# Kernel optimization log

Measured on AMD Instinct MI355X. Metric: run time of the kernel, lower is better.

Reference implementation:

```python
import jax, jax.numpy as jnp
import numpy as np

N, G, CIN, COUT, K, M, H, W = 4, 8, 256, 256, 3, 4, 32, 32


def setup_inputs() -> dict:
    key = jax.random.key(0)
    ks = jax.random.split(key, 12)
    s = 0.02
    return {
        "x": jax.random.normal(ks[0], (N, G, CIN, H, W), jnp.float32),
        # grouped 1x1 conv weights: (G, out_per_group, in_per_group)
        "wq": jax.random.normal(ks[1], (G, COUT, CIN), jnp.float32) * s,
        "wk": jax.random.normal(ks[2], (G, COUT, CIN), jnp.float32) * s,
        "wv": jax.random.normal(ks[3], (G, COUT, CIN), jnp.float32) * s,
        # relative embeddings: height varies over K1, width over K2
        "hm": jax.random.normal(ks[4], (G * COUT // 2, K, 1), jnp.float32),
        "wm": jax.random.normal(ks[5], (G * COUT // 2, 1, K), jnp.float32),
        "w_conv": jax.random.normal(ks[6], (G, CIN, COUT), jnp.float32) * s,
        "b_conv": jnp.zeros((G, CIN), jnp.float32),
        "w_f1": jax.random.normal(ks[7], (G, COUT, CIN), jnp.float32) * s,
        "b_f1": jnp.zeros((G, COUT), jnp.float32),
        "w_f2": jax.random.normal(ks[8], (G, CIN, COUT), jnp.float32) * s,
        "b_f2": jnp.zeros((G, CIN), jnp.float32),
        "g1": jnp.ones((CIN // M,), jnp.float32),
        "b1": jnp.zeros((CIN // M,), jnp.float32),
        "g2": jnp.ones((CIN // M,), jnp.float32),
        "b2": jnp.zeros((CIN // M,), jnp.float32),
    }


def _gconv(x, w, b=None):
    # grouped 1x1 conv: x (N,G,Ci,H,W), w (G,Co,Ci)
    y = jnp.einsum('ngihw,goi->ngohw', x, w)
    return y if b is None else y + b[None, :, :, None, None]


def _unfold(x4, k):
    # nn.Unfold(k, 1, (k-1)//2, 1): x4 (N,C,H,W) -> patches (N,C,k,k,H,W)
    p = (k - 1) // 2
    hh, ww = x4.shape[2], x4.shape[3]
    xp = jnp.pad(x4, ((0, 0), (0, 0), (p, p), (p, p)))
    return jnp.stack(
        [jnp.stack([xp[:, :, i:i + hh, j:j + ww] for j in range(k)], axis=2)
         for i in range(k)], axis=2)


def _skip(t, m):
    # 'N G (M D) H W -> N (H W) M G D'
    n, g, c, h, w = t.shape
    d = c // m
    return t.reshape(n, g, m, d, h, w).transpose(0, 4, 5, 2, 1, 3).reshape(n, h * w, m, g, d)


def _ln(t, gamma, beta, eps=1e-5):
    mu = t.mean(-1, keepdims=True)
    var = t.var(-1, keepdims=True)  # biased, matches torch LayerNorm
    return (t - mu) / jnp.sqrt(var + eps) * gamma + beta


def _forward(x, wq, wk, wv, hm, wm, w_conv, b_conv, w_f1, b_f1, w_f2, b_f2, g1, b1, g2, b2):
    n, g, c, h, w = x.shape
    m = M
    dout = COUT // m
    q = _gconv(x, wq).reshape(n, g, m, dout, h, w)
    k0 = _gconv(x, wk).reshape(n, g * COUT, h, w)
    kp = _unfold(k0, K)  # (n, G*COUT, K, K, h, w)
    half = g * COUT // 2
    kp = jnp.concatenate(
        [kp[:, :half] + hm[None, :, :, :, None, None],
         kp[:, half:] + wm[None, :, :, :, None, None]], axis=1)
    kp = kp.reshape(n, g, m, dout, K, K, h, w)
    v0 = _gconv(x, wv).reshape(n, g * COUT, h, w)
    vp = _unfold(v0, K).reshape(n, g, m, dout, K, K, h, w)
    # per (pixel, head): q (G,D) @ k (D, G*KK) -> softmax -> @ v (G*KK, D)
    scores = jnp.einsum('ngmdhw,nemdijhw->nhwmgeij', q, kp)
    attn = jax.nn.softmax(scores.reshape(n, h, w, m, g, -1), axis=-1)
    attn = attn.reshape(n, h, w, m, g, g, K, K)
    av = jnp.einsum('nhwmgeij,nemdijhw->ngmdhw', attn, vp)
    y = av.reshape(n, g, m * dout, h, w)
    y = _gconv(y, w_conv, b_conv)  # (n, g, CIN, h, w)
    t = _ln(_skip(x, m) + _skip(y, m), g1, b1)  # (n, hw, m, g, d)
    # NB: source does .reshape (not a permute) here -> intentional layout scramble
    y = t.reshape(n, g, -1, h, w)
    f = _gconv(jax.nn.relu(_gconv(y, w_f1, b_f1)), w_f2, b_f2)
    t2 = _ln(_skip(y, m) + _skip(f, m), g2, b2)
    return t2.reshape(n, g, -1, h, w)


def reference(x, wq, wk, wv, hm, wm, w_conv, b_conv, w_f1, b_f1, w_f2, b_f2, g1, b1, g2, b2):
    return _forward(x, wq, wk, wv, hm, wm, w_conv, b_conv, w_f1, b_f1, w_f2, b_f2, g1, b1, g2, b2)
```

## Files before the change

kernel.cpp:

```cpp
#include <hip/hip_runtime.h>


typedef unsigned short u16;
typedef unsigned int u32;
typedef __attribute__((ext_vector_type(8))) short bf16x8;
typedef __attribute__((ext_vector_type(4))) float f32x4;

__device__ __forceinline__ u32 fbits(float f) { u32 x; __builtin_memcpy(&x, &f, 4); return x; }
__device__ __forceinline__ float bf2f(u32 v) {
    u32 x = v << 16; float f; __builtin_memcpy(&f, &x, 4); return f;
}
__device__ __forceinline__ u16 f2bf(float f) {
    u32 x = fbits(f);
    u32 r = x + 0x7fffu + ((x >> 16) & 1u);
    return (u16)(r >> 16);
}
__device__ __forceinline__ u32 pack2bf(float a, float b) {
    return __builtin_amdgcn_perm(fbits(b) + 0x8000u, fbits(a) + 0x8000u, 0x07060302u);
}

__device__ __forceinline__ void unpack8(uint4 u, float* o) {
    o[0] = bf2f(u.x & 0xffff); o[1] = bf2f(u.x >> 16);
    o[2] = bf2f(u.y & 0xffff); o[3] = bf2f(u.y >> 16);
    o[4] = bf2f(u.z & 0xffff); o[5] = bf2f(u.z >> 16);
    o[6] = bf2f(u.w & 0xffff); o[7] = bf2f(u.w >> 16);
}
__device__ __forceinline__ void ld8bf(const u16* p, float* o) { unpack8(*(const uint4*)p, o); }
__device__ __forceinline__ void ld8f(const float* p, float* o) {
    float4 a = *(const float4*)p, b = *(const float4*)(p + 4);
    o[0] = a.x; o[1] = a.y; o[2] = a.z; o[3] = a.w;
    o[4] = b.x; o[5] = b.y; o[6] = b.z; o[7] = b.w;
}
__device__ __forceinline__ void st4bf(u16* p, const float* v) {
    ushort4 s; s.x = f2bf(v[0]); s.y = f2bf(v[1]); s.z = f2bf(v[2]); s.w = f2bf(v[3]);
    *(ushort4*)p = s;
}

#if defined(__has_builtin)
#if __has_builtin(__builtin_amdgcn_fdot2_f32_bf16)
#define HAVE_BFDOT 1
#endif
#endif
#ifdef HAVE_BFDOT
typedef __attribute__((ext_vector_type(2))) __bf16 v2bf;
__device__ __forceinline__ float dot2bf(u32 a, u32 b, float c) {
    return __builtin_amdgcn_fdot2_f32_bf16(__builtin_bit_cast(v2bf, a),
                                           __builtin_bit_cast(v2bf, b), c, false);
}
#else
__device__ __forceinline__ float dot2bf(u32 a, u32 b, float c) {
    return c + bf2f(a & 0xffff) * bf2f(b & 0xffff) + bf2f(a >> 16) * bf2f(b >> 16);
}
#endif
__device__ __forceinline__ float dot8bf(uint4 a, uint4 b, float c) {
    c = dot2bf(a.x, b.x, c); c = dot2bf(a.y, b.y, c);
    c = dot2bf(a.z, b.z, c); c = dot2bf(a.w, b.w, c);
    return c;
}

typedef const __attribute__((address_space(1))) u32 glob_u32;
typedef __attribute__((address_space(3))) u32 lds_u32;

__device__ __forceinline__ void gl16(const void* g, void* l) {
    __builtin_amdgcn_global_load_lds((glob_u32*)g, (lds_u32*)l, 16, 0, 0);
}

__global__ __launch_bounds__(256) void rel_kernel(const float* __restrict__ hm,
                                                  const float* __restrict__ wm,
                                                  u16* __restrict__ relT) {
    const int t = threadIdx.x;
    const int c0 = t << 3;
    const float* rb = (t < 128) ? (hm + (size_t)c0 * 3)
                                : (wm + (size_t)(c0 - 1024) * 3);
    float r[24];
    #pragma unroll
    for (int q = 0; q < 6; q++) {
        float4 f = *(const float4*)(rb + q * 4);
        r[q * 4] = f.x; r[q * 4 + 1] = f.y; r[q * 4 + 2] = f.z; r[q * 4 + 3] = f.w;
    }
    const int obase = ((c0 >> 6) & 3) * 512 + (c0 >> 8) * 64 + (c0 & 63);
    #pragma unroll
    for (int idx = 0; idx < 3; idx++) {
        u32 pk[4];
        #pragma unroll
        for (int j = 0; j < 4; j++)
            pk[j] = pack2bf(r[(2 * j) * 3 + idx], r[(2 * j + 1) * 3 + idx]);
        *(uint4*)(relT + idx * 2048 + obase) = *(uint4*)pk;
    }
}

template<int BMODE, int OM, int RELU, int RF32>
__global__ __launch_bounds__(256) void gemm_kernel(
    const float* __restrict__ A0, const float* __restrict__ A1,
    const float* __restrict__ A2, const void* __restrict__ B,
    const float* __restrict__ bias, const void* __restrict__ resid,
    const float* __restrict__ gamma, const float* __restrict__ beta,
    u16* __restrict__ O0, u16* __restrict__ O1, u16* __restrict__ O2) {
    __shared__ __align__(16) char smem[OM >= 2 ? 37376 : (OM == 1 ? 33792 : 20480)];
    u16* Al = (u16*)smem;
    u16* Bl = (u16*)(smem + 10240);
    float* Cl = (float*)smem;
    float* red  = (float*)(smem + 33792);
    float* mu_s = (float*)(smem + 35840);
    float* rs_s = (float*)(smem + 36352);
    float* g_s  = (float*)(smem + 36864);
    float* b_s  = (float*)(smem + 37120);

    const int tid = threadIdx.x;
    const int pt = blockIdx.x, ot = blockIdx.y;
    const int ngz = blockIdx.z, sel = ngz >> 5, ng = ngz & 31;
    const float* A = (sel == 0) ? A0 : (sel == 1) ? A1 : A2;
    u16* out      = (sel == 0) ? O0 : (sel == 1) ? O1 : O2;
    const int n = ng >> 3, g = ng & 7;
    const int p0 = pt << 7, o0 = ot << 7;
    const float* Ag = A + (size_t)g * 65536;

    if (OM >= 2 && tid < 64) { g_s[tid] = gamma[tid]; b_s[tid] = beta[tid]; }

    const int l = tid & 63, w = tid >> 6;
    const int mq = w >> 1;
    const int mw = mq << 6, nw = (w & 1) << 6;
    const int lrow = l & 15, lk = (l >> 4) << 3;

    f32x4 acc[4][4];
    #pragma unroll
    for (int i = 0; i < 4; i++)
        #pragma unroll
        for (int j = 0; j < 4; j++) acc[i][j] = (f32x4){0.f, 0.f, 0.f, 0.f};

    for (int k0 = 0; k0 < 256; k0 += 32) {
        {
            const int r = tid >> 1, cb = (tid & 1) << 4;
            const float* src = Ag + (size_t)(o0 + r) * 256 + k0 + cb;
            u32* dst = (u32*)&Al[r * 40 + cb];
            #pragma unroll
            for (int q = 0; q < 4; q++) {
                float4 f = *(const float4*)(src + q * 4);
                dst[q * 2]     = pack2bf(f.x, f.y);
                dst[q * 2 + 1] = pack2bf(f.z, f.w);
            }
        }
        if (BMODE == 2) {
            const int r = tid >> 1, cb = (tid & 1) << 4;
            const int k = k0 + cb;
            const int cmaj = ((k >> 6) << 9) + g * 64 + (k & 63);
            const u16* src = (const u16*)B + (size_t)(n * 1024 + p0 + r) * 2048 + cmaj;
            *(uint4*)&Bl[r * 40 + cb]     = *(const uint4*)src;
            *(uint4*)&Bl[r * 40 + cb + 8] = *(const uint4*)(src + 8);
        } else if (BMODE == 1) {
            const int kp = tid & 15, po = tid >> 4;
            const u16* src = (const u16*)B + (size_t)(ng * 256 + k0 + 2 * kp) * 1024 + p0 + po * 8;
            uint4 r0 = *(const uint4*)src;
            uint4 r1 = *(const uint4*)(src + 1024);
            u32 a0[4] = { r0.x, r0.y, r0.z, r0.w };
            u32 a1[4] = { r1.x, r1.y, r1.z, r1.w };
            #pragma unroll
            for (int j = 0; j < 4; j++) {
                u32 w0 = __builtin_amdgcn_perm(a1[j], a0[j], 0x05040100u);
                u32 w1 = __builtin_amdgcn_perm(a1[j], a0[j], 0x07060302u);
                *(u32*)&Bl[(po * 8 + 2 * j    ) * 40 + 2 * kp] = w0;
                *(u32*)&Bl[(po * 8 + 2 * j + 1) * 40 + 2 * kp] = w1;
            }
        } else {
            const int kp = tid & 15, po = tid >> 4;
            const float* src = (const float*)B + (size_t)(ng * 256 + k0 + 2 * kp) * 1024 + p0 + po * 8;
            float r0[8], r1[8];
            ld8f(src, r0); ld8f(src + 1024, r1);
            #pragma unroll
            for (int j = 0; j < 8; j++)
                *(u32*)&Bl[(po * 8 + j) * 40 + 2 * kp] = pack2bf(r0[j], r1[j]);
        }
        __syncthreads();
        bf16x8 af[4], bfg[4];
        #pragma unroll
        for (int i = 0; i < 4; i++) af[i]  = *(const bf16x8*)&Al[(mw + i * 16 + lrow) * 40 + lk];
        #pragma unroll
        for (int j = 0; j < 4; j++) bfg[j] = *(const bf16x8*)&Bl[(nw + j * 16 + lrow) * 40 + lk];
        #pragma unroll
        for (int i = 0; i < 4; i++)
            #pragma unroll
            for (int j = 0; j < 4; j++)
                acc[i][j] = __builtin_amdgcn_mfma_f32_16x16x32_bf16(af[i], bfg[j], acc[i][j], 0, 0, 0);
        __syncthreads();
    }

    if (OM == 0) {
        #pragma unroll
        for (int i = 0; i < 4; i++) {
            const int orow = o0 + mw + i * 16 + ((l >> 4) << 2);
            const int cmaj = ((orow >> 6) << 9) + g * 64 + (orow & 63);
            #pragma unroll
            for (int j = 0; j < 4; j++) {
                const int p = p0 + nw + j * 16 + lrow;
                float v4[4] = { acc[i][j].x, acc[i][j].y, acc[i][j].z, acc[i][j].w };
                st4bf(out + (size_t)(n * 1024 + p) * 2048 + cmaj, v4);
            }
        }
    } else if (OM == 1) {
        for (int ph = 0; ph < 2; ph++) {
            __syncthreads();
            if (mq == ph) {
                #pragma unroll
                for (int i = 0; i < 4; i++) {
                    const int rl = i * 16 + ((l >> 4) << 2);
                    #pragma unroll
                    for (int j = 0; j < 4; j++) {
                        const int c = nw + j * 16 + lrow;
                        Cl[(rl    ) * 132 + c] = acc[i][j].x;
                        Cl[(rl + 1) * 132 + c] = acc[i][j].y;
                        Cl[(rl + 2) * 132 + c] = acc[i][j].z;
                        Cl[(rl + 3) * 132 + c] = acc[i][j].w;
                    }
                }
            }
            __syncthreads();
            {
                const int row = tid >> 2, pc = (tid & 3) << 5;
                const int og = o0 + ph * 64 + row;
                const float bb = bias ? bias[g * 256 + og] : 0.f;
                u32 pk[16];
                #pragma unroll
                for (int q = 0; q < 8; q++) {
                    float4 f = *(const float4*)&Cl[row * 132 + pc + q * 4];
                    float a0 = f.x + bb, a1 = f.y + bb, a2 = f.z + bb, a3 = f.w + bb;
                    if (RELU) {
                        a0 = fmaxf(a0, 0.f); a1 = fmaxf(a1, 0.f);
                        a2 = fmaxf(a2, 0.f); a3 = fmaxf(a3, 0.f);
                    }
                    pk[q * 2]     = pack2bf(a0, a1);
                    pk[q * 2 + 1] = pack2bf(a2, a3);
                }
                u16* dst = out + (size_t)(ng * 256 + og) * 1024 + p0 + pc;
                #pragma unroll
                for (int q = 0; q < 4; q++) *(uint4*)(dst + q * 8) = *(uint4*)&pk[q * 4];
            }
        }
    } else {
        for (int ph = 0; ph < 2; ph++) {
            const int ms = (ot << 1) | ph;
            __syncthreads();
            if (mq == ph) {
                #pragma unroll
                for (int i = 0; i < 4; i++) {
                    const int rl = i * 16 + ((l >> 4) << 2);
                    #pragma unroll
                    for (int j = 0; j < 4; j++) {
                        const int c = nw + j * 16 + lrow;
                        Cl[(rl    ) * 132 + c] = acc[i][j].x;
                        Cl[(rl + 1) * 132 + c] = acc[i][j].y;
                        Cl[(rl + 2) * 132 + c] = acc[i][j].z;
                        Cl[(rl + 3) * 132 + c] = acc[i][j].w;
                    }
                }
            }
            __syncthreads();
            {
                const int row = tid >> 2, pc = (tid & 3) << 5;
                const int o = (ms << 6) + row;
                const float bb = bias[g * 256 + o];
                const size_t rb = (size_t)(ng * 256 + o) * 1024 + p0 + pc;
                float* cp = &Cl[row * 132 + pc];
                #pragma unroll
                for (int c8 = 0; c8 < 4; c8++) {
                    float r8[8];
                    if (RF32) ld8f((const float*)resid + rb + c8 * 8, r8);
                    else      ld8bf((const u16*)resid + rb + c8 * 8, r8);
                    #pragma unroll
                    for (int u = 0; u < 8; u++) cp[c8 * 8 + u] += bb + r8[u];
                }
            }
            __syncthreads();
            {
                const int c = tid & 127, hh = tid >> 7;
                float sm = 0.f, sq = 0.f;
                #pragma unroll
                for (int r = 0; r < 32; r++) {
                    float v = Cl[(hh * 32 + r) * 132 + c];
                    sm += v; sq += v * v;
                }
                red[hh * 128 + c] = sm; red[256 + hh * 128 + c] = sq;
            }
            __syncthreads();
            if (tid < 128) {
                float s2 = red[tid] + red[128 + tid];
                float q2 = red[256 + tid] + red[384 + tid];
                float mu = s2 * (1.f / 64.f);
                float var = q2 * (1.f / 64.f) - mu * mu;
                mu_s[tid] = mu; rs_s[tid] = rsqrtf(var + 1e-5f);
            }
            __syncthreads();
            {
                const int c = tid & 127, dh = (tid >> 7) << 5;
                const float mu = mu_s[c], rs = rs_s[c];
                const size_t ob = (size_t)n * 2097152 + (size_t)(p0 + c) * 2048
                                + ms * 512 + g * 64 + dh;
                if (OM == 3) {
                    float* op = (float*)O0 + ob;
                    #pragma unroll
                    for (int q4 = 0; q4 < 8; q4++) {
                        float4 f;
                        f.x = (Cl[(dh + q4 * 4    ) * 132 + c] - mu) * rs * g_s[dh + q4 * 4    ] + b_s[dh + q4 * 4    ];
                        f.y = (Cl[(dh + q4 * 4 + 1) * 132 + c] - mu) * rs * g_s[dh + q4 * 4 + 1] + b_s[dh + q4 * 4 + 1];
                        f.z = (Cl[(dh + q4 * 4 + 2) * 132 + c] - mu) * rs * g_s[dh + q4 * 4 + 2] + b_s[dh + q4 * 4 + 2];
                        f.w = (Cl[(dh + q4 * 4 + 3) * 132 + c] - mu) * rs * g_s[dh + q4 * 4 + 3] + b_s[dh + q4 * 4 + 3];
                        *(float4*)(op + q4 * 4) = f;
                    }
                } else {
                    u16* op = O0 + ob;
                    #pragma unroll
                    for (int q8 = 0; q8 < 4; q8++) {
                        u32 pk[4];
                        #pragma unroll
                        for (int j = 0; j < 4; j++) {
                            const int d = dh + q8 * 8 + j * 2;
                            float a = (Cl[(d    ) * 132 + c] - mu) * rs * g_s[d    ] + b_s[d    ];
                            float b = (Cl[(d + 1) * 132 + c] - mu) * rs * g_s[d + 1] + b_s[d + 1];
                            pk[j] = pack2bf(a, b);
                        }
                        *(uint4*)(op + q8 * 8) = *(uint4*)pk;
                    }
                }
            }
        }
    }
}

#define SBAR() __builtin_amdgcn_sched_barrier(0)
__global__ __launch_bounds__(256, 4) void attn_kernel(
    const u16* __restrict__ qt, const u16* __restrict__ kt,
    const u16* __restrict__ vt, const u16* __restrict__ relT,
    u16* __restrict__ av) {
    __shared__ __align__(16) char kvb[9 * 4096];
    const int tid = threadIdx.x;
    const int bx = blockIdx.x, n = blockIdx.y;
    const int p = ((bx & 7) << 7) | (bx >> 3);
    const int ph = p >> 5, pw = p & 31;
    const size_t nimg = (size_t)n * 1024;

    int cpix[9]; unsigned inb = 0;
    #pragma unroll
    for (int ij = 0; ij < 9; ij++) {
        int hs = ph + ij / 3 - 1, wc = pw + ij % 3 - 1;
        if (((unsigned)hs < 32u) && ((unsigned)wc < 32u)) inb |= (1u << ij);
        int hc = hs < 0 ? 0 : (hs > 31 ? 31 : hs);
        int wcl = wc < 0 ? 0 : (wc > 31 ? 31 : wc);
        cpix[ij] = hc * 32 + wcl;
    }

    const int e_th = tid & 7, g_th = (tid >> 3) & 7, m_th = tid >> 6;
    const int l = tid & 63;
    const int e_l = l >> 3, d8_l = l & 7;
    const int gsw = e_l * 64 + ((d8_l ^ e_l) & 7) * 8;
    char* ldst = kvb + m_th * 1024;
    const u16* kb = kt + nimg * 2048 + m_th * 512 + gsw;
    const u16* vb = vt + nimg * 2048 + m_th * 512 + gsw;

    uint4 qv[8];
    {
        const u16* qp = qt + (nimg + p) * 2048 + m_th * 512 + g_th * 64;
        #pragma unroll
        for (int c8 = 0; c8 < 8; c8++) qv[c8] = *(const uint4*)(qp + c8 * 8);
    }
    SBAR();
    #pragma unroll
    for (int idx = 0; idx < 3; idx++)
        gl16(relT + idx * 2048 + m_th * 512 + gsw, ldst + idx * 4096);
    SBAR();
    #pragma unroll
    for (int ij = 3; ij < 9; ij++)
        gl16(kb + (size_t)cpix[ij] * 2048, ldst + ij * 4096);
    SBAR();
    asm volatile("s_waitcnt vmcnt(6)" ::: "memory");
    SBAR();
    float qrel3[3] = {};
    const int qkb = m_th * 1024 + e_th * 128;
    #pragma unroll
    for (int c8 = 0; c8 < 8; c8++) {
        const int sw = ((c8 ^ e_th) & 7) << 4;
        #pragma unroll
        for (int idx = 0; idx < 3; idx++) {
            uint4 rv = *(const uint4*)(kvb + idx * 4096 + qkb + sw);
            qrel3[idx] = dot8bf(qv[c8], rv, qrel3[idx]);
        }
    }
    asm volatile("s_waitcnt lgkmcnt(0)" ::: "memory");
    SBAR();
    #pragma unroll
    for (int ij = 0; ij < 3; ij++)
        gl16(kb + (size_t)cpix[ij] * 2048, ldst + ij * 4096);
    SBAR();
    asm volatile("s_waitcnt vmcnt(3)" ::: "memory");
    SBAR();
    float sc[9] = {};
    #pragma unroll
    for (int c8 = 0; c8 < 8; c8++) {
        const int sw = ((c8 ^ e_th) & 7) << 4;
        #pragma unroll
        for (int ij = 3; ij < 9; ij++)
            if (inb & (1u << ij)) {
                uint4 kv = *(const uint4*)(kvb + ij * 4096 + qkb + sw);
                sc[ij] = dot8bf(qv[c8], kv, sc[ij]);
            }
    }
    asm volatile("s_waitcnt lgkmcnt(0)" ::: "memory");
    SBAR();
    #pragma unroll
    for (int ij = 3; ij < 9; ij++)
        gl16(vb + (size_t)cpix[ij] * 2048, ldst + ij * 4096);
    SBAR();
    asm volatile("s_waitcnt vmcnt(6)" ::: "memory");
    SBAR();
    #pragma unroll
    for (int c8 = 0; c8 < 8; c8++) {
        const int sw = ((c8 ^ e_th) & 7) << 4;
        #pragma unroll
        for (int ij = 0; ij < 3; ij++)
            if (inb & (1u << ij)) {
                uint4 kv = *(const uint4*)(kvb + ij * 4096 + qkb + sw);
                sc[ij] = dot8bf(qv[c8], kv, sc[ij]);
            }
    }
    asm volatile("s_waitcnt lgkmcnt(0)" ::: "memory");
    SBAR();
    #pragma unroll
    for (int ij = 0; ij < 3; ij++)
        gl16(vb + (size_t)cpix[ij] * 2048, ldst + ij * 4096);
    SBAR();

    #pragma unroll
    for (int ij = 0; ij < 9; ij++)
        sc[ij] += qrel3[(e_th < 4) ? (ij / 3) : (ij % 3)];

    float mx = sc[0];
    #pragma unroll
    for (int ij = 1; ij < 9; ij++) mx = fmaxf(mx, sc[ij]);
    mx = fmaxf(mx, __shfl_xor(mx, 1));
    mx = fmaxf(mx, __shfl_xor(mx, 2));
    mx = fmaxf(mx, __shfl_xor(mx, 4));
    float sum = 0.f;
    #pragma unroll
    for (int ij = 0; ij < 9; ij++) { sc[ij] = __expf(sc[ij] - mx); sum += sc[ij]; }
    sum += __shfl_xor(sum, 1); sum += __shfl_xor(sum, 2); sum += __shfl_xor(sum, 4);
    const float rinv = 1.f / sum;
    #pragma unroll
    for (int ij = 0; ij < 9; ij++) sc[ij] *= rinv;

    asm volatile("s_waitcnt vmcnt(0)" ::: "memory");
    SBAR();

    __builtin_amdgcn_s_setprio(1);
    const int db = l & 7, srcb = l & 0x38;
    const int avb = m_th * 1024;
    float acc[8] = {};
    #pragma unroll
    for (int ij = 0; ij < 9; ij++) {
        if (!(inb & (1u << ij))) continue;
        #pragma unroll
        for (int e = 0; e < 8; e++) {
            const float a = __shfl(sc[ij], srcb | e);
            uint4 vv = *(const uint4*)(kvb + ij * 4096 + avb + e * 128 + (((db ^ e) & 7) << 4));
            float v8[8];
            unpack8(vv, v8);
            #pragma unroll
            for (int u = 0; u < 8; u++) acc[u] += a * v8[u];
        }
    }
    __builtin_amdgcn_s_setprio(0);
    const int c0 = m_th * 512 + (l >> 3) * 64 + (l & 7) * 8;
    st4bf(av + (nimg + p) * 2048 + c0, acc);
    st4bf(av + (nimg + p) * 2048 + c0 + 4, acc + 4);
}
#undef SBAR

extern "C" void kernel_launch(void* const* d_in, const int* in_sizes, int n_in,
                              void* d_out, int out_size, void* d_ws, size_t ws_size,
                              hipStream_t stream) {
    const float* x   = (const float*)d_in[0];
    const float* wq  = (const float*)d_in[1];
    const float* wk  = (const float*)d_in[2];
    const float* wv  = (const float*)d_in[3];
    const float* hm  = (const float*)d_in[4];
    const float* wm  = (const float*)d_in[5];
    const float* wc  = (const float*)d_in[6];
    const float* bc  = (const float*)d_in[7];
    const float* wf1 = (const float*)d_in[8];
    const float* bf1 = (const float*)d_in[9];
    const float* wf2 = (const float*)d_in[10];
    const float* bf2w = (const float*)d_in[11];
    const float* g1  = (const float*)d_in[12];
    const float* b1  = (const float*)d_in[13];
    const float* g2  = (const float*)d_in[14];
    const float* b2  = (const float*)d_in[15];
    char* ws = (char*)d_ws;
    u16* bufQ = (u16*)d_out;
    u16* relT = bufQ + 8388608;
    u16* bufK = (u16*)(ws);
    u16* bufV = (u16*)(ws + 16777216);

    const dim3 gg(8, 2, 32), gq(8, 2, 96), gb(256);
    rel_kernel<<<dim3(1), gb, 0, stream>>>(hm, wm, relT);
    gemm_kernel<3, 0, 0, 0><<<gq, gb, 0, stream>>>(
        wq, wk, wv, x, nullptr, nullptr, nullptr, nullptr, bufQ, bufK, bufV);
    attn_kernel<<<dim3(1024, 4), gb, 0, stream>>>(bufQ, bufK, bufV, relT, bufQ);
    gemm_kernel<2, 2, 0, 1><<<gg, gb, 0, stream>>>(
        wc, wc, wc, bufQ, bc, x, g1, b1, bufV, bufV, bufV);
    gemm_kernel<1, 1, 1, 0><<<gg, gb, 0, stream>>>(
        wf1, wf1, wf1, bufV, bf1, nullptr, nullptr, nullptr, bufK, bufK, bufK);
    gemm_kernel<1, 3, 0, 0><<<gg, gb, 0, stream>>>(
        wf2, wf2, wf2, bufK, bf2w, bufV, g2, b2,
        (u16*)d_out, (u16*)d_out, (u16*)d_out);
}
```

Before: 318.5 us.

## Split attention neighbors into two online-softmax passes to shrink LDS footprint

The attention kernel's shared buffer shrinks from nine 4 KB slots to five, and the nine neighbors are processed in two chunks (5 then 4) using an online softmax that rescales the partial accumulator by the running max. Launch bounds go from 4 to 6 blocks per CU so the lower LDS use can turn into more resident blocks. The cost is extra serialization: more waits, a second round of K/V loads into reused slots, and the rescaling arithmetic, all of which reduce overlap within a block.

```diff
diff --git a/kernel.cpp b/kernel.cpp
--- a/kernel.cpp
+++ b/kernel.cpp
@@ -326,11 +326,11 @@
 }
 
 #define SBAR() __builtin_amdgcn_sched_barrier(0)
-__global__ __launch_bounds__(256, 4) void attn_kernel(
+__global__ __launch_bounds__(256, 6) void attn_kernel(
     const u16* __restrict__ qt, const u16* __restrict__ kt,
     const u16* __restrict__ vt, const u16* __restrict__ relT,
     u16* __restrict__ av) {
-    __shared__ __align__(16) char kvb[9 * 4096];
+    __shared__ __align__(16) char kvb[5 * 4096];
     const int tid = threadIdx.x;
     const int bx = blockIdx.x, n = blockIdx.y;
     const int p = ((bx & 7) << 7) | (bx >> 3);
@@ -354,6 +354,9 @@
     char* ldst = kvb + m_th * 1024;
     const u16* kb = kt + nimg * 2048 + m_th * 512 + gsw;
     const u16* vb = vt + nimg * 2048 + m_th * 512 + gsw;
+    const int qkb = m_th * 1024 + e_th * 128;
+    const int db = l & 7, srcb = l & 0x38;
+    const int avb = m_th * 1024;
 
     uint4 qv[8];
     {
@@ -366,14 +369,12 @@
     for (int idx = 0; idx < 3; idx++)
         gl16(relT + idx * 2048 + m_th * 512 + gsw, ldst + idx * 4096);
     SBAR();
-    #pragma unroll
-    for (int ij = 3; ij < 9; ij++)
-        gl16(kb + (size_t)cpix[ij] * 2048, ldst + ij * 4096);
-    SBAR();
-    asm volatile("s_waitcnt vmcnt(6)" ::: "memory");
+    gl16(kb + (size_t)cpix[3] * 2048, ldst + 3 * 4096);
+    gl16(kb + (size_t)cpix[4] * 2048, ldst + 4 * 4096);
+    SBAR();
+    asm volatile("s_waitcnt vmcnt(2)" ::: "memory");
     SBAR();
     float qrel3[3] = {};
-    const int qkb = m_th * 1024 + e_th * 128;
     #pragma unroll
     for (int c8 = 0; c8 < 8; c8++) {
         const int sw = ((c8 ^ e_th) & 7) << 4;
@@ -391,12 +392,12 @@
     SBAR();
     asm volatile("s_waitcnt vmcnt(3)" ::: "memory");
     SBAR();
-    float sc[9] = {};
+    float sc[5] = {};
     #pragma unroll
     for (int c8 = 0; c8 < 8; c8++) {
         const int sw = ((c8 ^ e_th) & 7) << 4;
         #pragma unroll
-        for (int ij = 3; ij < 9; ij++)
+        for (int ij = 3; ij < 5; ij++)
             if (inb & (1u << ij)) {
                 uint4 kv = *(const uint4*)(kvb + ij * 4096 + qkb + sw);
                 sc[ij] = dot8bf(qv[c8], kv, sc[ij]);
@@ -404,11 +405,10 @@
     }
     asm volatile("s_waitcnt lgkmcnt(0)" ::: "memory");
     SBAR();
-    #pragma unroll
-    for (int ij = 3; ij < 9; ij++)
-        gl16(vb + (size_t)cpix[ij] * 2048, ldst + ij * 4096);
-    SBAR();
-    asm volatile("s_waitcnt vmcnt(6)" ::: "memory");
+    gl16(vb + (size_t)cpix[3] * 2048, ldst + 3 * 4096);
+    gl16(vb + (size_t)cpix[4] * 2048, ldst + 4 * 4096);
+    SBAR();
+    asm volatile("s_waitcnt vmcnt(2)" ::: "memory");
     SBAR();
     #pragma unroll
     for (int c8 = 0; c8 < 8; c8++) {
@@ -426,34 +426,25 @@
     for (int ij = 0; ij < 3; ij++)
         gl16(vb + (size_t)cpix[ij] * 2048, ldst + ij * 4096);
     SBAR();
-
-    #pragma unroll
-    for (int ij = 0; ij < 9; ij++)
+    #pragma unroll
+    for (int ij = 0; ij < 5; ij++)
         sc[ij] += qrel3[(e_th < 4) ? (ij / 3) : (ij % 3)];
-
-    float mx = sc[0];
-    #pragma unroll
-    for (int ij = 1; ij < 9; ij++) mx = fmaxf(mx, sc[ij]);
-    mx = fmaxf(mx, __shfl_xor(mx, 1));
-    mx = fmaxf(mx, __shfl_xor(mx, 2));
-    mx = fmaxf(mx, __shfl_xor(mx, 4));
-    float sum = 0.f;
-    #pragma unroll
-    for (int ij = 0; ij < 9; ij++) { sc[ij] = __expf(sc[ij] - mx); sum += sc[ij]; }
-    sum += __shfl_xor(sum, 1); sum += __shfl_xor(sum, 2); sum += __shfl_xor(sum, 4);
-    const float rinv = 1.f / sum;
-    #pragma unroll
-    for (int ij = 0; ij < 9; ij++) sc[ij] *= rinv;
-
-    asm volatile("s_waitcnt vmcnt(0)" ::: "memory");
-    SBAR();
-
-    __builtin_amdgcn_s_setprio(1);
-    const int db = l & 7, srcb = l & 0x38;
-    const int avb = m_th * 1024;
+    float mA = sc[0];
+    #pragma unroll
+    for (int ij = 1; ij < 5; ij++) mA = fmaxf(mA, sc[ij]);
+    mA = fmaxf(mA, __shfl_xor(mA, 1));
+    mA = fmaxf(mA, __shfl_xor(mA, 2));
+    mA = fmaxf(mA, __shfl_xor(mA, 4));
+    float sA = 0.f;
+    #pragma unroll
+    for (int ij = 0; ij < 5; ij++) { sc[ij] = __expf(sc[ij] - mA); sA += sc[ij]; }
+    sA += __shfl_xor(sA, 1); sA += __shfl_xor(sA, 2); sA += __shfl_xor(sA, 4);
+
+    asm volatile("s_waitcnt vmcnt(3)" ::: "memory");
+    SBAR();
     float acc[8] = {};
     #pragma unroll
-    for (int ij = 0; ij < 9; ij++) {
+    for (int ij = 3; ij < 5; ij++) {
         if (!(inb & (1u << ij))) continue;
         #pragma unroll
         for (int e = 0; e < 8; e++) {
@@ -465,7 +456,87 @@
             for (int u = 0; u < 8; u++) acc[u] += a * v8[u];
         }
     }
+    asm volatile("s_waitcnt vmcnt(0)" ::: "memory");
+    SBAR();
+    #pragma unroll
+    for (int ij = 0; ij < 3; ij++) {
+        if (!(inb & (1u << ij))) continue;
+        #pragma unroll
+        for (int e = 0; e < 8; e++) {
+            const float a = __shfl(sc[ij], srcb | e);
+            uint4 vv = *(const uint4*)(kvb + ij * 4096 + avb + e * 128 + (((db ^ e) & 7) << 4));
+            float v8[8];
+            unpack8(vv, v8);
+            #pragma unroll
+            for (int u = 0; u < 8; u++) acc[u] += a * v8[u];
+        }
+    }
+    asm volatile("s_waitcnt lgkmcnt(0)" ::: "memory");
+    SBAR();
+    #pragma unroll
+    for (int t = 0; t < 4; t++)
+        gl16(kb + (size_t)cpix[5 + t] * 2048, ldst + t * 4096);
+    SBAR();
+    asm volatile("s_waitcnt vmcnt(0)" ::: "memory");
+    SBAR();
+    float scB[4] = {};
+    #pragma unroll
+    for (int c8 = 0; c8 < 8; c8++) {
+        const int sw = ((c8 ^ e_th) & 7) << 4;
+        #pragma unroll
+        for (int t = 0; t < 4; t++)
+            if (inb & (1u << (5 + t))) {
+                uint4 kv = *(const uint4*)(kvb + t * 4096 + qkb + sw);
+                scB[t] = dot8bf(qv[c8], kv, scB[t]);
+            }
+    }
+    asm volatile("s_waitcnt lgkmcnt(0)" ::: "memory");
+    SBAR();
+    #pragma unroll
+    for (int t = 0; t < 4; t++)
+        gl16(vb + (size_t)cpix[5 + t] * 2048, ldst + t * 4096);
+    SBAR();
+    #pragma unroll
+    for (int t = 0; t < 4; t++) {
+        const int ij = 5 + t;
+        scB[t] += qrel3[(e_th < 4) ? (ij / 3) : (ij % 3)];
+    }
+    float mB = scB[0];
+    #pragma unroll
+    for (int t = 1; t < 4; t++) mB = fmaxf(mB, scB[t]);
+    mB = fmaxf(mB, __shfl_xor(mB, 1));
+    mB = fmaxf(mB, __shfl_xor(mB, 2));
+    mB = fmaxf(mB, __shfl_xor(mB, 4));
+    const float m = fmaxf(mA, mB);
+    const float scaleA = __expf(mA - m);
+    #pragma unroll
+    for (int u = 0; u < 8; u++) acc[u] *= scaleA;
+    sA *= scaleA;
+    float sB = 0.f;
+    #pragma unroll
+    for (int t = 0; t < 4; t++) { scB[t] = __expf(scB[t] - m); sB += scB[t]; }
+    sB += __shfl_xor(sB, 1); sB += __shfl_xor(sB, 2); sB += __shfl_xor(sB, 4);
+    const float rinv = 1.f / (sA + sB);
+
+    asm volatile("s_waitcnt vmcnt(0)" ::: "memory");
+    SBAR();
+    __builtin_amdgcn_s_setprio(1);
+    #pragma unroll
+    for (int t = 0; t < 4; t++) {
+        if (!(inb & (1u << (5 + t)))) continue;
+        #pragma unroll
+        for (int e = 0; e < 8; e++) {
+            const float a = __shfl(scB[t], srcb | e);
+            uint4 vv = *(const uint4*)(kvb + t * 4096 + avb + e * 128 + (((db ^ e) & 7) << 4));
+            float v8[8];
+            unpack8(vv, v8);
+            #pragma unroll
+            for (int u = 0; u < 8; u++) acc[u] += a * v8[u];
+        }
+    }
     __builtin_amdgcn_s_setprio(0);
+    #pragma unroll
+    for (int u = 0; u < 8; u++) acc[u] *= rinv;
     const int c0 = m_th * 512 + (l >> 3) * 64 + (l & 7) * 8;
     st4bf(av + (nimg + p) * 2048 + c0, acc);
     st4bf(av + (nimg + p) * 2048 + c0 + 4, acc + 4);
```

Measured after the change: 501.7 us. 1.58x slower.
